# Kernel optimization log

Hardware: AMD Instinct MI355X
Metric: run time of the kernel (lower is better)

## Reference

```python
import jax, jax.numpy as jnp
import numpy as np

BELIEF = 1024
STOCH = 32
DISC = 32
LATENT = 1024
MLP = 1024
ACT = 6
B = 256
T = 64
UNIMIX = 0.01
FREE = 0.1
DYN_SCALE = 1.0
REP_SCALE = 0.1
EPS = 1e-8
SAMP_EPS = 1e-6
CLIP = 20.0
UPDATE_BIAS = -1.0


def _lin_init(key, fan_in, fan_out):
    return jax.random.normal(key, (fan_in, fan_out), jnp.float32) / np.sqrt(fan_in)


def setup_inputs() -> dict:
    key = jax.random.key(0)
    ks = jax.random.split(key, 16)
    inp = {
        "b0": jnp.zeros((B, BELIEF), jnp.float32),
        "z0": jax.random.uniform(ks[0], (B, STOCH * DISC), jnp.float32),
        "actions": jax.random.normal(ks[1], (T, B, ACT), jnp.float32),
        "obs": jax.random.normal(ks[2], (T, B, LATENT), jnp.float32),
        "u_noise": jax.random.uniform(ks[3], (T, B, STOCH, DISC), jnp.float32),
        # imagine_in MLP: (stoch*disc + act) -> MLP -> LATENT
        "Wi1": _lin_init(ks[4], STOCH * DISC + ACT, MLP),
        "bi1": jnp.zeros((MLP,), jnp.float32),
        "Wi2": _lin_init(ks[5], MLP, LATENT),
        "bi2": jnp.zeros((LATENT,), jnp.float32),
        # GRU linear: (LATENT + BELIEF) -> 3*BELIEF, no bias; LayerNorm(3*BELIEF, eps=1e-3)
        "Wg": _lin_init(ks[6], LATENT + BELIEF, 3 * BELIEF),
        "ln_scale": jnp.ones((3 * BELIEF,), jnp.float32),
        "ln_bias": jnp.zeros((3 * BELIEF,), jnp.float32),
        # posterior MLP: (LATENT + BELIEF) -> LATENT -> STOCH*DISC
        "Wo1": _lin_init(ks[7], LATENT + BELIEF, LATENT),
        "bo1": jnp.zeros((LATENT,), jnp.float32),
        "Wo2": _lin_init(ks[8], LATENT, STOCH * DISC),
        "bo2": jnp.zeros((STOCH * DISC,), jnp.float32),
        # prior (belief decoder) MLP: BELIEF -> LATENT -> STOCH*DISC
        "Wp1": _lin_init(ks[9], BELIEF, LATENT),
        "bp1": jnp.zeros((LATENT,), jnp.float32),
        "Wp2": _lin_init(ks[10], LATENT, STOCH * DISC),
        "bp2": jnp.zeros((STOCH * DISC,), jnp.float32),
    }
    return inp


def _mlp2(x, W1, b1, W2, b2):
    h = jax.nn.silu(x @ W1 + b1)
    return h @ W2 + b2


def _layernorm(x, scale, bias, eps=1e-3):
    mu = x.mean(-1, keepdims=True)
    var = ((x - mu) ** 2).mean(-1, keepdims=True)
    return (x - mu) / jnp.sqrt(var + eps) * scale + bias


def _probs_from_logits(logits_flat):
    # reshape (..., STOCH*DISC) -> (..., STOCH, DISC), clip, softmax, unimix
    logits = logits_flat.reshape(*logits_flat.shape[:-1], STOCH, DISC)
    logits = jnp.clip(logits, -CLIP, CLIP)
    probs = jax.nn.softmax(logits, axis=-1)
    probs = probs * (1.0 - UNIMIX) + UNIMIX / DISC
    return probs


def _kl_cate(post_probs, prior_probs):
    sg = jax.lax.stop_gradient
    log_post = jnp.log(post_probs + EPS)
    kl_rep = (post_probs * (log_post - jnp.log(sg(prior_probs) + EPS))).sum((-2, -1))
    kl_dyn = (sg(post_probs) * (sg(log_post) - jnp.log(prior_probs + EPS))).sum((-2, -1))
    rep_loss = jnp.maximum(kl_rep, FREE)
    dyn_loss = jnp.maximum(kl_dyn, FREE)
    return DYN_SCALE * dyn_loss + REP_SCALE * rep_loss


def reference(b0, z0, actions, obs, u_noise,
              Wi1, bi1, Wi2, bi2,
              Wg, ln_scale, ln_bias,
              Wo1, bo1, Wo2, bo2,
              Wp1, bp1, Wp2, bp2):
    def gru(inp, h):
        gates = _layernorm(jnp.concatenate([inp, h], axis=-1) @ Wg, ln_scale, ln_bias)
        r, c, u = jnp.split(gates, 3, axis=-1)
        reset = jax.nn.sigmoid(r)
        cand = jnp.tanh(reset * c)
        update = jax.nn.sigmoid(u + UPDATE_BIAS)
        return update * cand + (1.0 - update) * h

    def step(carry, xs):
        b, z = carry
        a_t, o_t, u_t = xs
        inp = _mlp2(jnp.concatenate([z, a_t], axis=-1), Wi1, bi1, Wi2, bi2)
        b_new = gru(inp, b)                                      # (B, BELIEF)
        prior_probs = _probs_from_logits(_mlp2(b_new, Wp1, bp1, Wp2, bp2))
        post_probs = _probs_from_logits(
            _mlp2(jnp.concatenate([o_t, b_new], axis=-1), Wo1, bo1, Wo2, bo2))
        # gumbel-max categorical sample + straight-through one-hot
        g = -jnp.log(-jnp.log(u_t + SAMP_EPS) + SAMP_EPS)
        logp = jnp.log(jnp.maximum(post_probs, SAMP_EPS))
        hard = jnp.argmax(logp + g, axis=-1)                     # (B, STOCH)
        y_hard = jax.nn.one_hot(hard, DISC, dtype=post_probs.dtype)
        z_st = y_hard + post_probs - jax.lax.stop_gradient(post_probs)
        z_flat = z_st.reshape(z_st.shape[0], STOCH * DISC)
        loss = _kl_cate(post_probs, prior_probs)                 # (B,)
        return (b_new, z_flat), loss

    (_, _), losses = jax.lax.scan(step, (b0, z0), (actions, obs, u_noise))
    return losses  # (T, B)
```

## Files before the change

kernel.cpp:

```cpp
#include <hip/hip_runtime.h>
#include <math.h>


typedef _Float16 f16;
typedef _Float16 f16x8 __attribute__((ext_vector_type(8)));
typedef float f32x4 __attribute__((ext_vector_type(4)));

constexpr int kB = 256, kN1 = 1024, kG3N = 3072, kActD = 6, kT = 64;
constexpr float kLoScale = 4096.f;
constexpr float kLoInv = 1.f / 4096.f;

__device__ __forceinline__ void wr_planes(f16* hi, f16* lo, size_t i, float x) {
  f16 h = (f16)x;
  hi[i] = h;
  lo[i] = (f16)((x - (float)h) * kLoScale);
}

__device__ __forceinline__ void glds16(const f16* g, f16* l) {
  __builtin_amdgcn_global_load_lds(
      (const __attribute__((address_space(1))) unsigned int*)g,
      (__attribute__((address_space(3))) unsigned int*)l, 16, 0, 0);
}

struct MJob {
  const f16 *A1h, *A1l, *A2h, *A2l;
  const f16 *Wph, *Wpl;
  float* outF;
  int cols1, K, Nout, k0, klen, ny;
};
struct MJobs { MJob j[6]; };

__global__ __launch_bounds__(256, 2) void k_mgemm(MJobs js) {
  const MJob jb = js.j[blockIdx.z];
  if ((int)blockIdx.y >= jb.ny) return;
  const int m0 = blockIdx.x * 128, n0 = blockIdx.y * 64;
  __shared__ __align__(16) f16 As[2][2][8][64][8];
  __shared__ __align__(16) f16 Ws[2][2][4][64][8];
  const int t = threadIdx.x, wave = t >> 6, lane = t & 63;
  const int rlo = lane & 15, khi = (lane >> 4) * 8;
  const int wmf = (wave & 1) * 4, wnf = (wave >> 1) * 2;

  f32x4 acc1[4][2], acc2[4][2];
#pragma unroll
  for (int i = 0; i < 4; ++i)
#pragma unroll
    for (int j = 0; j < 2; ++j)
#pragma unroll
      for (int r = 0; r < 4; ++r) { acc1[i][j][r] = 0.f; acc2[i][j][r] = 0.f; }

  auto issueTile = [&](int it, int buf) {
    const int kg = jb.k0 + it * 32;
    const f16 *h, *l; int rs, cb;
    if (kg < jb.cols1) { h = jb.A1h; l = jb.A1l; rs = jb.cols1; cb = kg; }
    else { h = jb.A2h; l = jb.A2l; rs = jb.K - jb.cols1; cb = kg - jb.cols1; }
#pragma unroll
    for (int i = 0; i < 2; ++i) {
      const int mf = wave * 2 + i;
      const size_t go = (size_t)(m0 + mf * 16 + rlo) * rs + cb + khi;
      glds16(h + go, &As[buf][0][mf][0][0]);
      glds16(l + go, &As[buf][1][mf][0][0]);
    }
    const size_t wo = (size_t)(n0 + wave * 16 + rlo) * jb.K + kg + khi;
    glds16(jb.Wph + wo, &Ws[buf][0][wave][0][0]);
    glds16(jb.Wpl + wo, &Ws[buf][1][wave][0][0]);
  };

  issueTile(0, 0);
  __syncthreads();
  const int niter = jb.klen >> 5;
  for (int it = 0; it < niter; ++it) {
    const int buf = it & 1;
    if (it + 1 < niter) issueTile(it + 1, buf ^ 1);
    f16x8 Af[4][2], Wf[2][2];
#pragma unroll
    for (int mf = 0; mf < 4; ++mf) {
      Af[mf][0] = *(const f16x8*)&As[buf][0][wmf + mf][lane][0];
      Af[mf][1] = *(const f16x8*)&As[buf][1][wmf + mf][lane][0];
    }
#pragma unroll
    for (int nf = 0; nf < 2; ++nf) {
      Wf[nf][0] = *(const f16x8*)&Ws[buf][0][wnf + nf][lane][0];
      Wf[nf][1] = *(const f16x8*)&Ws[buf][1][wnf + nf][lane][0];
    }
#pragma unroll
    for (int mf = 0; mf < 4; ++mf)
#pragma unroll
      for (int nf = 0; nf < 2; ++nf) {
        acc1[mf][nf] = __builtin_amdgcn_mfma_f32_16x16x32_f16(Af[mf][0], Wf[nf][0], acc1[mf][nf], 0, 0, 0);
        acc2[mf][nf] = __builtin_amdgcn_mfma_f32_16x16x32_f16(Af[mf][0], Wf[nf][1], acc2[mf][nf], 0, 0, 0);
        acc2[mf][nf] = __builtin_amdgcn_mfma_f32_16x16x32_f16(Af[mf][1], Wf[nf][0], acc2[mf][nf], 0, 0, 0);
      }
    __syncthreads();
  }
  const int orow = m0 + (wave & 1) * 64, ocol = n0 + (wave >> 1) * 32;
#pragma unroll
  for (int mf = 0; mf < 4; ++mf)
#pragma unroll
    for (int nf = 0; nf < 2; ++nf)
#pragma unroll
      for (int r = 0; r < 4; ++r) {
        const int row = orow + mf * 16 + (lane >> 4) * 4 + r;
        const int col = ocol + nf * 16 + rlo;
        jb.outF[(size_t)row * jb.Nout + col] = acc1[mf][nf][r] + acc2[mf][nf][r] * kLoInv;
      }
}

struct CJob { const float* P; int nparts; const float* bias; f16* oh; f16* ol; };
struct CJobs { CJob j[2]; };

__global__ __launch_bounds__(256) void k_comb(CJobs js) {
  const CJob jb = js.j[blockIdx.y];
  const int i = blockIdx.x * 256 + threadIdx.x;
  float s = 0.f;
  for (int p = 0; p < jb.nparts; ++p) s += jb.P[(size_t)p * (kB * kN1) + i];
  s += jb.bias[i & (kN1 - 1)];
  s = s * (1.f / (1.f + expf(-s)));
  wr_planes(jb.oh, jb.ol, i, s);
}

__global__ __launch_bounds__(256) void k_conv(const float* src, f16* dh, f16* dl) {
  const size_t i = (size_t)blockIdx.x * 256 + threadIdx.x;
  wr_planes(dh, dl, i, src[i]);
}

__global__ __launch_bounds__(256) void k_convT(const float* src, int rowoff, int srcN,
                                               int K, f16* dh, f16* dl) {
  __shared__ float T[64][65];
  const int k0 = blockIdx.x * 64, n0 = blockIdx.y * 64;
  const int tx = threadIdx.x & 63, ty = threadIdx.x >> 6;
#pragma unroll 4
  for (int i = 0; i < 16; ++i) {
    const int k = ty * 16 + i;
    T[k][tx] = src[(size_t)(rowoff + k0 + k) * srcN + n0 + tx];
  }
  __syncthreads();
#pragma unroll 4
  for (int i = 0; i < 16; ++i) {
    const int n = ty * 16 + i;
    const float x = T[tx][n];
    const size_t o = (size_t)(n0 + n) * K + k0 + tx;
    f16 h = (f16)x;
    dh[o] = h;
    dl[o] = (f16)((x - (float)h) * kLoScale);
  }
}

__global__ __launch_bounds__(256) void k_bfused(const float* Wg, const float* bi2, float* bf) {
  const int n = blockIdx.x * 256 + threadIdx.x;
  float s = 0.f;
  for (int j = 0; j < 1024; ++j) s += bi2[j] * Wg[(size_t)j * kG3N + n];
  bf[n] = s;
}

__global__ __launch_bounds__(256) void k_setup(const float* b0, float* bbuf, f16* bh, f16* bl) {
  const size_t i = (size_t)blockIdx.x * 256 + threadIdx.x;
  const float b = b0[i];
  bbuf[i] = b;
  wr_planes(bh, bl, i, b);
}

__global__ __launch_bounds__(256) void k_finish0(const float* P, const float* Wi1,
    const float* bi1, const float* act0, f16* h1h, f16* h1l) {
  const int b = blockIdx.y;
  const int j = blockIdx.x * 256 + threadIdx.x;
  __shared__ float sact[kActD];
  if (threadIdx.x < kActD) sact[threadIdx.x] = act0[b * kActD + threadIdx.x];
  __syncthreads();
  float s = P[(size_t)b * kN1 + j] + bi1[j];
#pragma unroll
  for (int k = 0; k < kActD; ++k) s += sact[k] * Wi1[(size_t)(kN1 + k) * kN1 + j];
  s = s * (1.f / (1.f + expf(-s)));
  wr_planes(h1h, h1l, (size_t)b * kN1 + j, s);
}

__global__ __launch_bounds__(256) void k_gru(const float* Pg, const float* bfused,
    const float* lns, const float* lnb, float* bbuf, f16* bh, f16* bl,
    const float* obs_next, f16* oh, f16* ol, int do_obs) {
  const int b = blockIdx.x;
  const int tid = threadIdx.x;
  const size_t S3 = (size_t)kB * kG3N;
  __shared__ float sh[kG3N];
  __shared__ float red[8];
  float v[12];
  float sum = 0.f, sq = 0.f;
#pragma unroll
  for (int i = 0; i < 12; ++i) {
    const int j = tid + i * 256;
    const size_t o = (size_t)b * kG3N + j;
    const float s = Pg[o] + Pg[S3 + o] + Pg[2 * S3 + o] + Pg[3 * S3 + o] + bfused[j];
    v[i] = s; sum += s; sq += s * s;
  }
  if (do_obs) {
#pragma unroll
    for (int i = 0; i < 4; ++i) {
      const int j = tid + i * 256;
      wr_planes(oh, ol, (size_t)b * kN1 + j, obs_next[(size_t)b * kN1 + j]);
    }
  }
  for (int m = 1; m <= 32; m <<= 1) { sum += __shfl_xor(sum, m); sq += __shfl_xor(sq, m); }
  if ((tid & 63) == 0) { red[(tid >> 6) * 2] = sum; red[(tid >> 6) * 2 + 1] = sq; }
  __syncthreads();
  float ts = 0.f, tq = 0.f;
  for (int w = 0; w < 4; ++w) { ts += red[w * 2]; tq += red[w * 2 + 1]; }
  const float mu   = ts * (1.f / kG3N);
  const float var  = tq * (1.f / kG3N) - mu * mu;
  const float rinv = 1.f / sqrtf(var + 1e-3f);
#pragma unroll
  for (int i = 0; i < 12; ++i) {
    const int j = tid + i * 256;
    sh[j] = (v[i] - mu) * rinv * lns[j] + lnb[j];
  }
  __syncthreads();
#pragma unroll
  for (int i = 0; i < 4; ++i) {
    const int j = tid + i * 256;
    const float r = sh[j], c = sh[kN1 + j], u = sh[2 * kN1 + j];
    const float reset = 1.f / (1.f + expf(-r));
    const float cand  = tanhf(reset * c);
    const float upd   = 1.f / (1.f + expf(-(u - 1.f)));
    const size_t o = (size_t)b * kN1 + j;
    const float bn = upd * cand + (1.f - upd) * bbuf[o];
    bbuf[o] = bn;
    wr_planes(bh, bl, o, bn);
  }
}

__global__ __launch_bounds__(1024) void k_sample(const float* PE,
    const float* bp2, const float* bo2, const float* unz_t, float* loss_t,
    const float* Wi1, const float* bi1, const float* act_next,
    f16* h1h, f16* h1l, int do_gather) {
  const int b = blockIdx.x;
  const int tid = threadIdx.x;
  const size_t PL = (size_t)kB * kN1;
  const size_t o = (size_t)b * kN1 + tid;
  float lp = PE[o] + PE[PL + o] + bp2[tid];
  float lo = PE[2 * PL + o] + PE[3 * PL + o] + bo2[tid];
  lp = fminf(fmaxf(lp, -20.f), 20.f);
  lo = fminf(fmaxf(lo, -20.f), 20.f);
  float mp = lp, mo = lo;
  for (int m = 1; m <= 16; m <<= 1) { mp = fmaxf(mp, __shfl_xor(mp, m)); mo = fmaxf(mo, __shfl_xor(mo, m)); }
  const float ep = expf(lp - mp), eo = expf(lo - mo);
  float sp = ep, so = eo;
  for (int m = 1; m <= 16; m <<= 1) { sp += __shfl_xor(sp, m); so += __shfl_xor(so, m); }
  const float pp = (ep / sp) * 0.99f + (0.01f / 32.f);
  const float po = (eo / so) * 0.99f + (0.01f / 32.f);
  float kt = po * (logf(po + 1e-8f) - logf(pp + 1e-8f));
  for (int m = 1; m <= 16; m <<= 1) kt += __shfl_xor(kt, m);
  const float u = unz_t[o];
  const float g = -logf(-logf(u + 1e-6f) + 1e-6f);
  float vv = logf(fmaxf(po, 1e-6f)) + g;
  int ii = tid & 31;
  for (int m = 1; m <= 16; m <<= 1) {
    const float vo = __shfl_xor(vv, m);
    const int   io = __shfl_xor(ii, m);
    if (vo > vv || (vo == vv && io < ii)) { vv = vo; ii = io; }
  }
  __shared__ float skl[32];
  __shared__ int   sidx[32];
  if ((tid & 31) == 0) { skl[tid >> 5] = kt; sidx[tid >> 5] = ii; }
  __syncthreads();
  if (tid == 0) {
    float kl = 0.f;
    for (int gg = 0; gg < 32; ++gg) kl += skl[gg];
    const float dl = fmaxf(kl, 0.1f);
    loss_t[b] = 1.0f * dl + 0.1f * dl;
  }
  if (do_gather) {
    float s = bi1[tid];
#pragma unroll
    for (int gg = 0; gg < 32; ++gg)
      s += Wi1[(size_t)(gg * 32 + sidx[gg]) * kN1 + tid];
#pragma unroll
    for (int k = 0; k < kActD; ++k)
      s += act_next[b * kActD + k] * Wi1[(size_t)(kN1 + k) * kN1 + tid];
    s = s * (1.f / (1.f + expf(-s)));
    wr_planes(h1h, h1l, o, s);
  }
}

extern "C" void kernel_launch(void* const* d_in, const int* in_sizes, int n_in,
                              void* d_out, int out_size, void* d_ws, size_t ws_size,
                              hipStream_t stream) {
  const float* b0   = (const float*)d_in[0];
  const float* z0   = (const float*)d_in[1];
  const float* acts = (const float*)d_in[2];
  const float* obs  = (const float*)d_in[3];
  const float* unz  = (const float*)d_in[4];
  const float* Wi1  = (const float*)d_in[5];
  const float* bi1  = (const float*)d_in[6];
  const float* Wi2  = (const float*)d_in[7];
  const float* bi2  = (const float*)d_in[8];
  const float* Wg   = (const float*)d_in[9];
  const float* lns  = (const float*)d_in[10];
  const float* lnb  = (const float*)d_in[11];
  const float* Wo1  = (const float*)d_in[12];
  const float* bo1  = (const float*)d_in[13];
  const float* Wo2  = (const float*)d_in[14];
  const float* bo2  = (const float*)d_in[15];
  const float* Wp1  = (const float*)d_in[16];
  const float* bp1  = (const float*)d_in[17];
  const float* Wp2  = (const float*)d_in[18];
  const float* bp2  = (const float*)d_in[19];
  float* out = (float*)d_out;

  char* wsb = (char*)d_ws;
  size_t off = 0;
  auto allocB = [&](size_t bytes) { char* p = wsb + off; off += (bytes + 255) & ~(size_t)255; return p; };
  const size_t PL = (size_t)kB * kN1;
  const size_t S3 = (size_t)kB * kG3N;
  const size_t W1 = (size_t)kN1 * kN1;

  float* Pg = (float*)allocB(4 * S3 * 4);
  float* Wfused_tmp = Pg;
  f16* WgTh = (f16*)allocB(W1 * 3 * 2);
  f16* WgTl = (f16*)allocB(W1 * 3 * 2);
  float* PD = (float*)WgTh;
  float* PE = (float*)WgTl;
  f16* h1h = (f16*)allocB(PL * 2);  f16* h1l = (f16*)allocB(PL * 2);
  f16* bh  = (f16*)allocB(PL * 2);  f16* bl  = (f16*)allocB(PL * 2);
  f16* hph = (f16*)allocB(PL * 2);  f16* hpl = (f16*)allocB(PL * 2);
  f16* hoh = (f16*)allocB(PL * 2);  f16* hol = (f16*)allocB(PL * 2);
  f16* o0h = (f16*)allocB(PL * 2);  f16* o0l = (f16*)allocB(PL * 2);
  f16* o1h = (f16*)allocB(PL * 2);  f16* o1l = (f16*)allocB(PL * 2);
  f16* z0h = (f16*)allocB(PL * 2);  f16* z0l = (f16*)allocB(PL * 2);
  float* bbuf   = (float*)allocB(PL * 4);
  float* bfused = (float*)allocB((size_t)kG3N * 4);
  f16* WfTh = (f16*)allocB(W1 * 3 * 2);  f16* WfTl = (f16*)allocB(W1 * 3 * 2);
  f16* WgBh = (f16*)allocB(W1 * 3 * 2);  f16* WgBl = (f16*)allocB(W1 * 3 * 2);
  f16* Wi2h = (f16*)allocB(W1 * 2);      f16* Wi2l = (f16*)allocB(W1 * 2);
  f16* Wi1Th = (f16*)allocB(W1 * 2);     f16* Wi1Tl = (f16*)allocB(W1 * 2);
  f16* Wo1Th = (f16*)allocB(W1 * 2 * 2); f16* Wo1Tl = (f16*)allocB(W1 * 2 * 2);
  f16* Wp1Th = (f16*)allocB(W1 * 2);     f16* Wp1Tl = (f16*)allocB(W1 * 2);
  f16* Wp2Th = (f16*)allocB(W1 * 2);     f16* Wp2Tl = (f16*)allocB(W1 * 2);
  f16* Wo2Th = (f16*)allocB(W1 * 2);     f16* Wo2Tl = (f16*)allocB(W1 * 2);

  k_convT<<<dim3(16, 48), 256, 0, stream>>>(Wg, 0, kG3N, 1024, WgTh, WgTl);
  k_convT<<<dim3(16, 48), 256, 0, stream>>>(Wg, 1024, kG3N, 1024, WgBh, WgBl);
  k_convT<<<dim3(16, 16), 256, 0, stream>>>(Wi1, 0, kN1, 1024, Wi1Th, Wi1Tl);
  k_convT<<<dim3(32, 16), 256, 0, stream>>>(Wo1, 0, kN1, 2048, Wo1Th, Wo1Tl);
  k_convT<<<dim3(16, 16), 256, 0, stream>>>(Wp1, 0, kN1, 1024, Wp1Th, Wp1Tl);
  k_convT<<<dim3(16, 16), 256, 0, stream>>>(Wp2, 0, kN1, 1024, Wp2Th, Wp2Tl);
  k_convT<<<dim3(16, 16), 256, 0, stream>>>(Wo2, 0, kN1, 1024, Wo2Th, Wo2Tl);
  k_conv<<<dim3(4096), 256, 0, stream>>>(Wi2, Wi2h, Wi2l);
  k_bfused<<<dim3(12), 256, 0, stream>>>(Wg, bi2, bfused);
  {
    MJobs J{};
    J.j[0] = { Wi2h, Wi2l, nullptr, nullptr, WgTh, WgTl, Wfused_tmp, 1024, 1024, kG3N, 0, 1024, 48 };
    k_mgemm<<<dim3(8, 48, 1), 256, 0, stream>>>(J);
  }
  k_convT<<<dim3(16, 48), 256, 0, stream>>>(Wfused_tmp, 0, kG3N, 1024, WfTh, WfTl);
  k_setup<<<dim3(1024), 256, 0, stream>>>(b0, bbuf, bh, bl);
  k_conv<<<dim3(1024), 256, 0, stream>>>(z0, z0h, z0l);
  k_conv<<<dim3(1024), 256, 0, stream>>>(obs, o0h, o0l);
  {
    MJobs J{};
    J.j[0] = { z0h, z0l, nullptr, nullptr, Wi1Th, Wi1Tl, PD, 1024, 1024, kN1, 0, 1024, 16 };
    k_mgemm<<<dim3(2, 16, 1), 256, 0, stream>>>(J);
  }
  k_finish0<<<dim3(4, kB), 256, 0, stream>>>(PD, Wi1, bi1, acts, h1h, h1l);

  for (int t = 0; t < kT; ++t) {
    const float* unz_t = unz + (size_t)t * kB * kN1;
    f16* oth = (t & 1) ? o1h : o0h;
    f16* otl = (t & 1) ? o1l : o0l;
    f16* onh = (t & 1) ? o0h : o1h;
    f16* onl = (t & 1) ? o0l : o1l;

    {
      MJobs J{};
      J.j[0] = { h1h, h1l, nullptr, nullptr, WfTh, WfTl, Pg,          1024, 1024, kG3N, 0,   512, 48 };
      J.j[1] = { h1h, h1l, nullptr, nullptr, WfTh, WfTl, Pg + S3,     1024, 1024, kG3N, 512, 512, 48 };
      J.j[2] = { bh,  bl,  nullptr, nullptr, WgBh, WgBl, Pg + 2 * S3, 1024, 1024, kG3N, 0,   512, 48 };
      J.j[3] = { bh,  bl,  nullptr, nullptr, WgBh, WgBl, Pg + 3 * S3, 1024, 1024, kG3N, 512, 512, 48 };
      k_mgemm<<<dim3(2, 48, 4), 256, 0, stream>>>(J);
    }
    k_gru<<<dim3(kB), 256, 0, stream>>>(Pg, bfused, lns, lnb, bbuf, bh, bl,
                                        obs + (size_t)(t + 1) * kB * kN1, onh, onl,
                                        (t < kT - 1) ? 1 : 0);
    {
      MJobs J{};
      J.j[0] = { bh,  bl,  nullptr, nullptr, Wp1Th, Wp1Tl, PD,          1024, 1024, kN1, 0,    512, 16 };
      J.j[1] = { bh,  bl,  nullptr, nullptr, Wp1Th, Wp1Tl, PD + PL,     1024, 1024, kN1, 512,  512, 16 };
      J.j[2] = { oth, otl, bh, bl,           Wo1Th, Wo1Tl, PD + 2 * PL, 1024, 2048, kN1, 0,    512, 16 };
      J.j[3] = { oth, otl, bh, bl,           Wo1Th, Wo1Tl, PD + 3 * PL, 1024, 2048, kN1, 512,  512, 16 };
      J.j[4] = { oth, otl, bh, bl,           Wo1Th, Wo1Tl, PD + 4 * PL, 1024, 2048, kN1, 1024, 512, 16 };
      J.j[5] = { oth, otl, bh, bl,           Wo1Th, Wo1Tl, PD + 5 * PL, 1024, 2048, kN1, 1536, 512, 16 };
      k_mgemm<<<dim3(2, 16, 6), 256, 0, stream>>>(J);
    }
    {
      CJobs C{};
      C.j[0] = { PD,          2, bp1, hph, hpl };
      C.j[1] = { PD + 2 * PL, 4, bo1, hoh, hol };
      k_comb<<<dim3(1024, 2), 256, 0, stream>>>(C);
    }
    {
      MJobs J{};
      J.j[0] = { hph, hpl, nullptr, nullptr, Wp2Th, Wp2Tl, PE,          1024, 1024, kN1, 0,   512, 16 };
      J.j[1] = { hph, hpl, nullptr, nullptr, Wp2Th, Wp2Tl, PE + PL,     1024, 1024, kN1, 512, 512, 16 };
      J.j[2] = { hoh, hol, nullptr, nullptr, Wo2Th, Wo2Tl, PE + 2 * PL, 1024, 1024, kN1, 0,   512, 16 };
      J.j[3] = { hoh, hol, nullptr, nullptr, Wo2Th, Wo2Tl, PE + 3 * PL, 1024, 1024, kN1, 512, 512, 16 };
      k_mgemm<<<dim3(2, 16, 4), 256, 0, stream>>>(J);
    }
    k_sample<<<dim3(kB), 1024, 0, stream>>>(PE, bp2, bo2, unz_t,
                                            out + (size_t)t * kB,
                                            Wi1, bi1, acts + (size_t)(t + 1) * kB * kActD,
                                            h1h, h1l, (t < kT - 1) ? 1 : 0);
  }
}
```

Baseline: 5.980 ms.

## Fuse the per-timestep kernel sequence into one persistent kernel with grid barriers

Replaces the 64×6 per-step kernel launches (GEMMs, GRU, combine, sample) with a single persistent kernel. Its blocks loop over tasks for each stage and meet at a software grid-wide barrier built on an atomic counter. This removes launch overhead and inter-kernel gaps, and the block count is sized from occupancy. The cost is a spin barrier that needs every block co-resident, with a guard timeout that could silently break ordering. The sample stage now runs with 256 threads per batch row instead of 1024.

```diff
diff --git a/kernel.cpp b/kernel.cpp
--- a/kernel.cpp
+++ b/kernel.cpp
@@ -20,6 +20,304 @@
   __builtin_amdgcn_global_load_lds(
       (const __attribute__((address_space(1))) unsigned int*)g,
       (__attribute__((address_space(3))) unsigned int*)l, 16, 0, 0);
+}
+
+struct GemmLDS { f16 As[2][2][8][64][8]; f16 Ws[2][2][4][64][8]; };
+struct GruLDS  { float sh[kG3N]; float red[8]; };
+struct SmpLDS  { float skl[32]; int sidx[32]; };
+union ScanLDS  { GemmLDS g; GruLDS r; SmpLDS s; };
+
+__device__ void dev_mgemm(GemmLDS& L, const f16* A1h, const f16* A1l,
+                          const f16* A2h, const f16* A2l,
+                          const f16* Wph, const f16* Wpl, float* outF,
+                          int cols1, int K, int Nout, int k0, int klen,
+                          int bx, int by) {
+  const int m0 = bx * 128, n0 = by * 64;
+  const int tid = threadIdx.x, wave = tid >> 6, lane = tid & 63;
+  const int rlo = lane & 15, khi = (lane >> 4) * 8;
+  const int wmf = (wave & 1) * 4, wnf = (wave >> 1) * 2;
+
+  f32x4 acc1[4][2], acc2[4][2];
+#pragma unroll
+  for (int i = 0; i < 4; ++i)
+#pragma unroll
+    for (int j = 0; j < 2; ++j)
+#pragma unroll
+      for (int r = 0; r < 4; ++r) { acc1[i][j][r] = 0.f; acc2[i][j][r] = 0.f; }
+
+  auto issueTile = [&](int it, int buf) {
+    const int kg = k0 + it * 32;
+    const f16 *h, *l; int rs, cb;
+    if (kg < cols1) { h = A1h; l = A1l; rs = cols1; cb = kg; }
+    else { h = A2h; l = A2l; rs = K - cols1; cb = kg - cols1; }
+#pragma unroll
+    for (int i = 0; i < 2; ++i) {
+      const int mf = wave * 2 + i;
+      const size_t go = (size_t)(m0 + mf * 16 + rlo) * rs + cb + khi;
+      glds16(h + go, &L.As[buf][0][mf][0][0]);
+      glds16(l + go, &L.As[buf][1][mf][0][0]);
+    }
+    const size_t wo = (size_t)(n0 + wave * 16 + rlo) * K + kg + khi;
+    glds16(Wph + wo, &L.Ws[buf][0][wave][0][0]);
+    glds16(Wpl + wo, &L.Ws[buf][1][wave][0][0]);
+  };
+
+  issueTile(0, 0);
+  __syncthreads();
+  const int niter = klen >> 5;
+#pragma unroll 1
+  for (int it = 0; it < niter; ++it) {
+    const int buf = it & 1;
+    if (it + 1 < niter) issueTile(it + 1, buf ^ 1);
+    f16x8 Af[4][2], Wf[2][2];
+#pragma unroll
+    for (int mf = 0; mf < 4; ++mf) {
+      Af[mf][0] = *(const f16x8*)&L.As[buf][0][wmf + mf][lane][0];
+      Af[mf][1] = *(const f16x8*)&L.As[buf][1][wmf + mf][lane][0];
+    }
+#pragma unroll
+    for (int nf = 0; nf < 2; ++nf) {
+      Wf[nf][0] = *(const f16x8*)&L.Ws[buf][0][wnf + nf][lane][0];
+      Wf[nf][1] = *(const f16x8*)&L.Ws[buf][1][wnf + nf][lane][0];
+    }
+#pragma unroll
+    for (int mf = 0; mf < 4; ++mf)
+#pragma unroll
+      for (int nf = 0; nf < 2; ++nf) {
+        acc1[mf][nf] = __builtin_amdgcn_mfma_f32_16x16x32_f16(Af[mf][0], Wf[nf][0], acc1[mf][nf], 0, 0, 0);
+        acc2[mf][nf] = __builtin_amdgcn_mfma_f32_16x16x32_f16(Af[mf][0], Wf[nf][1], acc2[mf][nf], 0, 0, 0);
+        acc2[mf][nf] = __builtin_amdgcn_mfma_f32_16x16x32_f16(Af[mf][1], Wf[nf][0], acc2[mf][nf], 0, 0, 0);
+      }
+    __syncthreads();
+  }
+  const int orow = m0 + (wave & 1) * 64, ocol = n0 + (wave >> 1) * 32;
+#pragma unroll
+  for (int mf = 0; mf < 4; ++mf)
+#pragma unroll
+    for (int nf = 0; nf < 2; ++nf)
+#pragma unroll
+      for (int r = 0; r < 4; ++r) {
+        const int row = orow + mf * 16 + (lane >> 4) * 4 + r;
+        const int col = ocol + nf * 16 + rlo;
+        outF[(size_t)row * Nout + col] = acc1[mf][nf][r] + acc2[mf][nf][r] * kLoInv;
+      }
+}
+
+__device__ void dev_gru(GruLDS& G, int b, const float* Pg, const float* bfused,
+                        const float* lns, const float* lnb, float* bbuf,
+                        f16* bh, f16* bl, const float* obs_next,
+                        f16* oh, f16* ol, int do_obs) {
+  const int tid = threadIdx.x;
+  const size_t S3 = (size_t)kB * kG3N;
+  float v[12];
+  float sum = 0.f, sq = 0.f;
+#pragma unroll
+  for (int i = 0; i < 12; ++i) {
+    const int j = tid + i * 256;
+    const size_t o = (size_t)b * kG3N + j;
+    const float s = Pg[o] + Pg[S3 + o] + Pg[2 * S3 + o] + Pg[3 * S3 + o] + bfused[j];
+    v[i] = s; sum += s; sq += s * s;
+  }
+  if (do_obs) {
+#pragma unroll
+    for (int i = 0; i < 4; ++i) {
+      const int j = tid + i * 256;
+      wr_planes(oh, ol, (size_t)b * kN1 + j, obs_next[(size_t)b * kN1 + j]);
+    }
+  }
+  for (int m = 1; m <= 32; m <<= 1) { sum += __shfl_xor(sum, m); sq += __shfl_xor(sq, m); }
+  if ((tid & 63) == 0) { G.red[(tid >> 6) * 2] = sum; G.red[(tid >> 6) * 2 + 1] = sq; }
+  __syncthreads();
+  float ts = 0.f, tq = 0.f;
+  for (int w = 0; w < 4; ++w) { ts += G.red[w * 2]; tq += G.red[w * 2 + 1]; }
+  const float mu   = ts * (1.f / kG3N);
+  const float var  = tq * (1.f / kG3N) - mu * mu;
+  const float rinv = 1.f / sqrtf(var + 1e-3f);
+#pragma unroll
+  for (int i = 0; i < 12; ++i) {
+    const int j = tid + i * 256;
+    G.sh[j] = (v[i] - mu) * rinv * lns[j] + lnb[j];
+  }
+  __syncthreads();
+#pragma unroll
+  for (int i = 0; i < 4; ++i) {
+    const int j = tid + i * 256;
+    const float r = G.sh[j], c = G.sh[kN1 + j], u = G.sh[2 * kN1 + j];
+    const float reset = 1.f / (1.f + expf(-r));
+    const float cand  = tanhf(reset * c);
+    const float upd   = 1.f / (1.f + expf(-(u - 1.f)));
+    const size_t o = (size_t)b * kN1 + j;
+    const float bn = upd * cand + (1.f - upd) * bbuf[o];
+    bbuf[o] = bn;
+    wr_planes(bh, bl, o, bn);
+  }
+}
+
+__device__ void dev_sample(SmpLDS& S, int b, const float* PE,
+                           const float* bp2, const float* bo2,
+                           const float* unz_t, float* loss_t,
+                           const float* Wi1, const float* bi1,
+                           const float* act_next, f16* h1h, f16* h1l,
+                           int do_gather) {
+  const int tid = threadIdx.x;
+  const size_t PL = (size_t)kB * kN1;
+  __syncthreads();
+#pragma unroll
+  for (int c = 0; c < 4; ++c) {
+    const int j = c * 256 + tid;
+    const size_t o = (size_t)b * kN1 + j;
+    float lp = PE[o] + PE[PL + o] + bp2[j];
+    float lo = PE[2 * PL + o] + PE[3 * PL + o] + bo2[j];
+    lp = fminf(fmaxf(lp, -20.f), 20.f);
+    lo = fminf(fmaxf(lo, -20.f), 20.f);
+    float mp = lp, mo = lo;
+    for (int m = 1; m <= 16; m <<= 1) { mp = fmaxf(mp, __shfl_xor(mp, m)); mo = fmaxf(mo, __shfl_xor(mo, m)); }
+    const float ep = expf(lp - mp), eo = expf(lo - mo);
+    float sp = ep, so = eo;
+    for (int m = 1; m <= 16; m <<= 1) { sp += __shfl_xor(sp, m); so += __shfl_xor(so, m); }
+    const float pp = (ep / sp) * 0.99f + (0.01f / 32.f);
+    const float po = (eo / so) * 0.99f + (0.01f / 32.f);
+    float kt = po * (logf(po + 1e-8f) - logf(pp + 1e-8f));
+    for (int m = 1; m <= 16; m <<= 1) kt += __shfl_xor(kt, m);
+    const float u = unz_t[o];
+    const float g = -logf(-logf(u + 1e-6f) + 1e-6f);
+    float vv = logf(fmaxf(po, 1e-6f)) + g;
+    int ii = j & 31;
+    for (int m = 1; m <= 16; m <<= 1) {
+      const float vo = __shfl_xor(vv, m);
+      const int   io = __shfl_xor(ii, m);
+      if (vo > vv || (vo == vv && io < ii)) { vv = vo; ii = io; }
+    }
+    if ((tid & 31) == 0) { S.skl[j >> 5] = kt; S.sidx[j >> 5] = ii; }
+  }
+  __syncthreads();
+  if (tid == 0) {
+    float kl = 0.f;
+    for (int gg = 0; gg < 32; ++gg) kl += S.skl[gg];
+    const float dl = fmaxf(kl, 0.1f);
+    loss_t[b] = 1.0f * dl + 0.1f * dl;
+  }
+  if (do_gather) {
+#pragma unroll
+    for (int c = 0; c < 4; ++c) {
+      const int j = c * 256 + tid;
+      float s = bi1[j];
+#pragma unroll
+      for (int gg = 0; gg < 32; ++gg)
+        s += Wi1[(size_t)(gg * 32 + S.sidx[gg]) * kN1 + j];
+#pragma unroll
+      for (int k = 0; k < kActD; ++k)
+        s += act_next[b * kActD + k] * Wi1[(size_t)(kN1 + k) * kN1 + j];
+      s = s * (1.f / (1.f + expf(-s)));
+      wr_planes(h1h, h1l, (size_t)b * kN1 + j, s);
+    }
+  }
+}
+
+struct ScanArgs {
+  const float *obs, *acts, *unz;
+  float* out;
+  const float *lns, *lnb, *bp1, *bo1, *bp2, *bo2, *Wi1, *bi1;
+  float *Pg, *PD, *PE, *bbuf, *bfused;
+  const f16 *WfTh, *WfTl, *WgBh, *WgBl;
+  const f16 *Wp1Th, *Wp1Tl, *Wo1Th, *Wo1Tl, *Wp2Th, *Wp2Tl, *Wo2Th, *Wo2Tl;
+  f16 *h1h, *h1l, *bh, *bl, *hph, *hpl, *hoh, *hol, *o0h, *o0l, *o1h, *o1l;
+  int* cnt;
+  int NB;
+};
+
+__device__ __forceinline__ void gsync_impl(int* cnt, int tgt) {
+  __syncthreads();
+  if (threadIdx.x == 0) {
+    __threadfence();
+    __hip_atomic_fetch_add(cnt, 1, __ATOMIC_RELEASE, __HIP_MEMORY_SCOPE_AGENT);
+    int guard = 0;
+    while (__hip_atomic_load(cnt, __ATOMIC_RELAXED, __HIP_MEMORY_SCOPE_AGENT) < tgt) {
+      __builtin_amdgcn_s_sleep(2);
+      if (++guard > (1 << 26)) break;
+    }
+    __threadfence();
+  }
+  __syncthreads();
+}
+
+__global__ __launch_bounds__(256, 2) void k_scan(ScanArgs a) {
+  __shared__ ScanLDS L;
+  const int NB = a.NB;
+  const size_t PL = (size_t)kB * kN1;
+  const size_t S3 = (size_t)kB * kG3N;
+  int syncno = 0;
+
+#pragma unroll 1
+  for (int t = 0; t < kT; ++t) {
+    const f16* oth = (t & 1) ? a.o1h : a.o0h;
+    const f16* otl = (t & 1) ? a.o1l : a.o0l;
+    f16* onh = (t & 1) ? a.o0h : a.o1h;
+    f16* onl = (t & 1) ? a.o0l : a.o1l;
+
+#pragma unroll 1
+    for (int task = blockIdx.x; task < 384; task += NB) {
+      const int j = task / 96, r = task % 96, bx = r & 1, by = r >> 1;
+      const bool top = (j < 2);
+      dev_mgemm(L.g, top ? a.h1h : a.bh, top ? a.h1l : a.bl, nullptr, nullptr,
+                top ? a.WfTh : a.WgBh, top ? a.WfTl : a.WgBl,
+                a.Pg + (size_t)j * S3, 1024, 1024, kG3N, (j & 1) * 512, 512, bx, by);
+    }
+    gsync_impl(a.cnt, ++syncno * NB);
+
+#pragma unroll 1
+    for (int b = blockIdx.x; b < kB; b += NB)
+      dev_gru(L.r, b, a.Pg, a.bfused, a.lns, a.lnb, a.bbuf, a.bh, a.bl,
+              a.obs + (size_t)(t + 1) * kB * kN1, onh, onl, (t < kT - 1) ? 1 : 0);
+    gsync_impl(a.cnt, ++syncno * NB);
+
+#pragma unroll 1
+    for (int task = blockIdx.x; task < 192; task += NB) {
+      const int j = task >> 5, r = task & 31, bx = r & 1, by = r >> 1;
+      const f16 *Ah, *Al, *A2h = nullptr, *A2l = nullptr, *Wh, *Wl;
+      int K, k0;
+      if (j < 2) { Ah = a.bh; Al = a.bl; Wh = a.Wp1Th; Wl = a.Wp1Tl; K = 1024; k0 = j * 512; }
+      else { Ah = oth; Al = otl; A2h = a.bh; A2l = a.bl; Wh = a.Wo1Th; Wl = a.Wo1Tl; K = 2048; k0 = (j - 2) * 512; }
+      dev_mgemm(L.g, Ah, Al, A2h, A2l, Wh, Wl,
+                a.PD + (size_t)j * PL, 1024, K, kN1, k0, 512, bx, by);
+    }
+    gsync_impl(a.cnt, ++syncno * NB);
+
+#pragma unroll 1
+    for (int idx = blockIdx.x; idx < 2048; idx += NB) {
+      const int by = idx >> 10;
+      const int i = (idx & 1023) * 256 + (int)threadIdx.x;
+      const float* P = by ? (a.PD + 2 * PL) : a.PD;
+      const int np = by ? 4 : 2;
+      const float* bias = by ? a.bo1 : a.bp1;
+      f16* oh = by ? a.hoh : a.hph;
+      f16* ol = by ? a.hol : a.hpl;
+      float s = 0.f;
+      for (int p = 0; p < np; ++p) s += P[(size_t)p * PL + i];
+      s += bias[i & (kN1 - 1)];
+      s = s * (1.f / (1.f + expf(-s)));
+      wr_planes(oh, ol, i, s);
+    }
+    gsync_impl(a.cnt, ++syncno * NB);
+
+#pragma unroll 1
+    for (int task = blockIdx.x; task < 128; task += NB) {
+      const int j = task >> 5, r = task & 31, bx = r & 1, by = r >> 1;
+      const bool pr = (j < 2);
+      dev_mgemm(L.g, pr ? a.hph : a.hoh, pr ? a.hpl : a.hol, nullptr, nullptr,
+                pr ? a.Wp2Th : a.Wo2Th, pr ? a.Wp2Tl : a.Wo2Tl,
+                a.PE + (size_t)j * PL, 1024, 1024, kN1, (j & 1) * 512, 512, bx, by);
+    }
+    gsync_impl(a.cnt, ++syncno * NB);
+
+#pragma unroll 1
+    for (int b = blockIdx.x; b < kB; b += NB)
+      dev_sample(L.s, b, a.PE, a.bp2, a.bo2, a.unz + (size_t)t * PL,
+                 a.out + (size_t)t * kB, a.Wi1, a.bi1,
+                 a.acts + (size_t)(t + 1) * kB * kActD, a.h1h, a.h1l,
+                 (t < kT - 1) ? 1 : 0);
+    gsync_impl(a.cnt, ++syncno * NB);
+  }
 }
 
 struct MJob {
@@ -33,89 +331,9 @@
 __global__ __launch_bounds__(256, 2) void k_mgemm(MJobs js) {
   const MJob jb = js.j[blockIdx.z];
   if ((int)blockIdx.y >= jb.ny) return;
-  const int m0 = blockIdx.x * 128, n0 = blockIdx.y * 64;
-  __shared__ __align__(16) f16 As[2][2][8][64][8];
-  __shared__ __align__(16) f16 Ws[2][2][4][64][8];
-  const int t = threadIdx.x, wave = t >> 6, lane = t & 63;
-  const int rlo = lane & 15, khi = (lane >> 4) * 8;
-  const int wmf = (wave & 1) * 4, wnf = (wave >> 1) * 2;
-
-  f32x4 acc1[4][2], acc2[4][2];
-#pragma unroll
-  for (int i = 0; i < 4; ++i)
-#pragma unroll
-    for (int j = 0; j < 2; ++j)
-#pragma unroll
-      for (int r = 0; r < 4; ++r) { acc1[i][j][r] = 0.f; acc2[i][j][r] = 0.f; }
-
-  auto issueTile = [&](int it, int buf) {
-    const int kg = jb.k0 + it * 32;
-    const f16 *h, *l; int rs, cb;
-    if (kg < jb.cols1) { h = jb.A1h; l = jb.A1l; rs = jb.cols1; cb = kg; }
-    else { h = jb.A2h; l = jb.A2l; rs = jb.K - jb.cols1; cb = kg - jb.cols1; }
-#pragma unroll
-    for (int i = 0; i < 2; ++i) {
-      const int mf = wave * 2 + i;
-      const size_t go = (size_t)(m0 + mf * 16 + rlo) * rs + cb + khi;
-      glds16(h + go, &As[buf][0][mf][0][0]);
-      glds16(l + go, &As[buf][1][mf][0][0]);
-    }
-    const size_t wo = (size_t)(n0 + wave * 16 + rlo) * jb.K + kg + khi;
-    glds16(jb.Wph + wo, &Ws[buf][0][wave][0][0]);
-    glds16(jb.Wpl + wo, &Ws[buf][1][wave][0][0]);
-  };
-
-  issueTile(0, 0);
-  __syncthreads();
-  const int niter = jb.klen >> 5;
-  for (int it = 0; it < niter; ++it) {
-    const int buf = it & 1;
-    if (it + 1 < niter) issueTile(it + 1, buf ^ 1);
-    f16x8 Af[4][2], Wf[2][2];
-#pragma unroll
-    for (int mf = 0; mf < 4; ++mf) {
-      Af[mf][0] = *(const f16x8*)&As[buf][0][wmf + mf][lane][0];
-      Af[mf][1] = *(const f16x8*)&As[buf][1][wmf + mf][lane][0];
-    }
-#pragma unroll
-    for (int nf = 0; nf < 2; ++nf) {
-      Wf[nf][0] = *(const f16x8*)&Ws[buf][0][wnf + nf][lane][0];
-      Wf[nf][1] = *(const f16x8*)&Ws[buf][1][wnf + nf][lane][0];
-    }
-#pragma unroll
-    for (int mf = 0; mf < 4; ++mf)
-#pragma unroll
-      for (int nf = 0; nf < 2; ++nf) {
-        acc1[mf][nf] = __builtin_amdgcn_mfma_f32_16x16x32_f16(Af[mf][0], Wf[nf][0], acc1[mf][nf], 0, 0, 0);
-        acc2[mf][nf] = __builtin_amdgcn_mfma_f32_16x16x32_f16(Af[mf][0], Wf[nf][1], acc2[mf][nf], 0, 0, 0);
-        acc2[mf][nf] = __builtin_amdgcn_mfma_f32_16x16x32_f16(Af[mf][1], Wf[nf][0], acc2[mf][nf], 0, 0, 0);
-      }
-    __syncthreads();
-  }
-  const int orow = m0 + (wave & 1) * 64, ocol = n0 + (wave >> 1) * 32;
-#pragma unroll
-  for (int mf = 0; mf < 4; ++mf)
-#pragma unroll
-    for (int nf = 0; nf < 2; ++nf)
-#pragma unroll
-      for (int r = 0; r < 4; ++r) {
-        const int row = orow + mf * 16 + (lane >> 4) * 4 + r;
-        const int col = ocol + nf * 16 + rlo;
-        jb.outF[(size_t)row * jb.Nout + col] = acc1[mf][nf][r] + acc2[mf][nf][r] * kLoInv;
-      }
-}
-
-struct CJob { const float* P; int nparts; const float* bias; f16* oh; f16* ol; };
-struct CJobs { CJob j[2]; };
-
-__global__ __launch_bounds__(256) void k_comb(CJobs js) {
-  const CJob jb = js.j[blockIdx.y];
-  const int i = blockIdx.x * 256 + threadIdx.x;
-  float s = 0.f;
-  for (int p = 0; p < jb.nparts; ++p) s += jb.P[(size_t)p * (kB * kN1) + i];
-  s += jb.bias[i & (kN1 - 1)];
-  s = s * (1.f / (1.f + expf(-s)));
-  wr_planes(jb.oh, jb.ol, i, s);
+  __shared__ GemmLDS L;
+  dev_mgemm(L, jb.A1h, jb.A1l, jb.A2h, jb.A2l, jb.Wph, jb.Wpl, jb.outF,
+            jb.cols1, jb.K, jb.Nout, jb.k0, jb.klen, blockIdx.x, blockIdx.y);
 }
 
 __global__ __launch_bounds__(256) void k_conv(const float* src, f16* dh, f16* dl) {
@@ -159,6 +377,10 @@
   wr_planes(bh, bl, i, b);
 }
 
+__global__ void k_zero(int* p) {
+  if (threadIdx.x == 0 && blockIdx.x == 0) *p = 0;
+}
+
 __global__ __launch_bounds__(256) void k_finish0(const float* P, const float* Wi1,
     const float* bi1, const float* act0, f16* h1h, f16* h1l) {
   const int b = blockIdx.y;
@@ -171,111 +393,6 @@
   for (int k = 0; k < kActD; ++k) s += sact[k] * Wi1[(size_t)(kN1 + k) * kN1 + j];
   s = s * (1.f / (1.f + expf(-s)));
   wr_planes(h1h, h1l, (size_t)b * kN1 + j, s);
-}
-
-__global__ __launch_bounds__(256) void k_gru(const float* Pg, const float* bfused,
-    const float* lns, const float* lnb, float* bbuf, f16* bh, f16* bl,
-    const float* obs_next, f16* oh, f16* ol, int do_obs) {
-  const int b = blockIdx.x;
-  const int tid = threadIdx.x;
-  const size_t S3 = (size_t)kB * kG3N;
-  __shared__ float sh[kG3N];
-  __shared__ float red[8];
-  float v[12];
-  float sum = 0.f, sq = 0.f;
-#pragma unroll
-  for (int i = 0; i < 12; ++i) {
-    const int j = tid + i * 256;
-    const size_t o = (size_t)b * kG3N + j;
-    const float s = Pg[o] + Pg[S3 + o] + Pg[2 * S3 + o] + Pg[3 * S3 + o] + bfused[j];
-    v[i] = s; sum += s; sq += s * s;
-  }
-  if (do_obs) {
-#pragma unroll
-    for (int i = 0; i < 4; ++i) {
-      const int j = tid + i * 256;
-      wr_planes(oh, ol, (size_t)b * kN1 + j, obs_next[(size_t)b * kN1 + j]);
-    }
-  }
-  for (int m = 1; m <= 32; m <<= 1) { sum += __shfl_xor(sum, m); sq += __shfl_xor(sq, m); }
-  if ((tid & 63) == 0) { red[(tid >> 6) * 2] = sum; red[(tid >> 6) * 2 + 1] = sq; }
-  __syncthreads();
-  float ts = 0.f, tq = 0.f;
-  for (int w = 0; w < 4; ++w) { ts += red[w * 2]; tq += red[w * 2 + 1]; }
-  const float mu   = ts * (1.f / kG3N);
-  const float var  = tq * (1.f / kG3N) - mu * mu;
-  const float rinv = 1.f / sqrtf(var + 1e-3f);
-#pragma unroll
-  for (int i = 0; i < 12; ++i) {
-    const int j = tid + i * 256;
-    sh[j] = (v[i] - mu) * rinv * lns[j] + lnb[j];
-  }
-  __syncthreads();
-#pragma unroll
-  for (int i = 0; i < 4; ++i) {
-    const int j = tid + i * 256;
-    const float r = sh[j], c = sh[kN1 + j], u = sh[2 * kN1 + j];
-    const float reset = 1.f / (1.f + expf(-r));
-    const float cand  = tanhf(reset * c);
-    const float upd   = 1.f / (1.f + expf(-(u - 1.f)));
-    const size_t o = (size_t)b * kN1 + j;
-    const float bn = upd * cand + (1.f - upd) * bbuf[o];
-    bbuf[o] = bn;
-    wr_planes(bh, bl, o, bn);
-  }
-}
-
-__global__ __launch_bounds__(1024) void k_sample(const float* PE,
-    const float* bp2, const float* bo2, const float* unz_t, float* loss_t,
-    const float* Wi1, const float* bi1, const float* act_next,
-    f16* h1h, f16* h1l, int do_gather) {
-  const int b = blockIdx.x;
-  const int tid = threadIdx.x;
-  const size_t PL = (size_t)kB * kN1;
-  const size_t o = (size_t)b * kN1 + tid;
-  float lp = PE[o] + PE[PL + o] + bp2[tid];
-  float lo = PE[2 * PL + o] + PE[3 * PL + o] + bo2[tid];
-  lp = fminf(fmaxf(lp, -20.f), 20.f);
-  lo = fminf(fmaxf(lo, -20.f), 20.f);
-  float mp = lp, mo = lo;
-  for (int m = 1; m <= 16; m <<= 1) { mp = fmaxf(mp, __shfl_xor(mp, m)); mo = fmaxf(mo, __shfl_xor(mo, m)); }
-  const float ep = expf(lp - mp), eo = expf(lo - mo);
-  float sp = ep, so = eo;
-  for (int m = 1; m <= 16; m <<= 1) { sp += __shfl_xor(sp, m); so += __shfl_xor(so, m); }
-  const float pp = (ep / sp) * 0.99f + (0.01f / 32.f);
-  const float po = (eo / so) * 0.99f + (0.01f / 32.f);
-  float kt = po * (logf(po + 1e-8f) - logf(pp + 1e-8f));
-  for (int m = 1; m <= 16; m <<= 1) kt += __shfl_xor(kt, m);
-  const float u = unz_t[o];
-  const float g = -logf(-logf(u + 1e-6f) + 1e-6f);
-  float vv = logf(fmaxf(po, 1e-6f)) + g;
-  int ii = tid & 31;
-  for (int m = 1; m <= 16; m <<= 1) {
-    const float vo = __shfl_xor(vv, m);
-    const int   io = __shfl_xor(ii, m);
-    if (vo > vv || (vo == vv && io < ii)) { vv = vo; ii = io; }
-  }
-  __shared__ float skl[32];
-  __shared__ int   sidx[32];
-  if ((tid & 31) == 0) { skl[tid >> 5] = kt; sidx[tid >> 5] = ii; }
-  __syncthreads();
-  if (tid == 0) {
-    float kl = 0.f;
-    for (int gg = 0; gg < 32; ++gg) kl += skl[gg];
-    const float dl = fmaxf(kl, 0.1f);
-    loss_t[b] = 1.0f * dl + 0.1f * dl;
-  }
-  if (do_gather) {
-    float s = bi1[tid];
-#pragma unroll
-    for (int gg = 0; gg < 32; ++gg)
-      s += Wi1[(size_t)(gg * 32 + sidx[gg]) * kN1 + tid];
-#pragma unroll
-    for (int k = 0; k < kActD; ++k)
-      s += act_next[b * kActD + k] * Wi1[(size_t)(kN1 + k) * kN1 + tid];
-    s = s * (1.f / (1.f + expf(-s)));
-    wr_planes(h1h, h1l, o, s);
-  }
 }
 
 extern "C" void kernel_launch(void* const* d_in, const int* in_sizes, int n_in,
@@ -333,6 +450,24 @@
   f16* Wp1Th = (f16*)allocB(W1 * 2);     f16* Wp1Tl = (f16*)allocB(W1 * 2);
   f16* Wp2Th = (f16*)allocB(W1 * 2);     f16* Wp2Tl = (f16*)allocB(W1 * 2);
   f16* Wo2Th = (f16*)allocB(W1 * 2);     f16* Wo2Tl = (f16*)allocB(W1 * 2);
+  int* cnt = (int*)allocB(256);
+
+  static int s_nb = 0;
+  if (s_nb == 0) {
+    int dev = 0;
+    (void)hipGetDevice(&dev);
+    int cu = 0;
+    if (hipDeviceGetAttribute(&cu, hipDeviceAttributeMultiprocessorCount, dev) != hipSuccess || cu <= 0)
+      cu = 256;
+    int occ = 0;
+    if (hipOccupancyMaxActiveBlocksPerMultiprocessor(&occ, k_scan, 256, 0) != hipSuccess || occ < 1)
+      occ = 1;
+    long nb = (long)occ * (long)cu;
+    if (nb > 512) nb = 512;
+    if (nb < 64) nb = 64;
+    s_nb = (int)nb;
+  }
+  const int NB = s_nb;
 
   k_convT<<<dim3(16, 48), 256, 0, stream>>>(Wg, 0, kG3N, 1024, WgTh, WgTl);
   k_convT<<<dim3(16, 48), 256, 0, stream>>>(Wg, 1024, kG3N, 1024, WgBh, WgBl);
@@ -352,6 +487,7 @@
   k_setup<<<dim3(1024), 256, 0, stream>>>(b0, bbuf, bh, bl);
   k_conv<<<dim3(1024), 256, 0, stream>>>(z0, z0h, z0l);
   k_conv<<<dim3(1024), 256, 0, stream>>>(obs, o0h, o0l);
+  k_zero<<<dim3(1), 64, 0, stream>>>(cnt);
   {
     MJobs J{};
     J.j[0] = { z0h, z0l, nullptr, nullptr, Wi1Th, Wi1Tl, PD, 1024, 1024, kN1, 0, 1024, 16 };
@@ -359,51 +495,17 @@
   }
   k_finish0<<<dim3(4, kB), 256, 0, stream>>>(PD, Wi1, bi1, acts, h1h, h1l);
 
-  for (int t = 0; t < kT; ++t) {
-    const float* unz_t = unz + (size_t)t * kB * kN1;
-    f16* oth = (t & 1) ? o1h : o0h;
-    f16* otl = (t & 1) ? o1l : o0l;
-    f16* onh = (t & 1) ? o0h : o1h;
-    f16* onl = (t & 1) ? o0l : o1l;
-
-    {
-      MJobs J{};
-      J.j[0] = { h1h, h1l, nullptr, nullptr, WfTh, WfTl, Pg,          1024, 1024, kG3N, 0,   512, 48 };
-      J.j[1] = { h1h, h1l, nullptr, nullptr, WfTh, WfTl, Pg + S3,     1024, 1024, kG3N, 512, 512, 48 };
-      J.j[2] = { bh,  bl,  nullptr, nullptr, WgBh, WgBl, Pg + 2 * S3, 1024, 1024, kG3N, 0,   512, 48 };
-      J.j[3] = { bh,  bl,  nullptr, nullptr, WgBh, WgBl, Pg + 3 * S3, 1024, 1024, kG3N, 512, 512, 48 };
-      k_mgemm<<<dim3(2, 48, 4), 256, 0, stream>>>(J);
-    }
-    k_gru<<<dim3(kB), 256, 0, stream>>>(Pg, bfused, lns, lnb, bbuf, bh, bl,
-                                        obs + (size_t)(t + 1) * kB * kN1, onh, onl,
-                                        (t < kT - 1) ? 1 : 0);
-    {
-      MJobs J{};
-      J.j[0] = { bh,  bl,  nullptr, nullptr, Wp1Th, Wp1Tl, PD,          1024, 1024, kN1, 0,    512, 16 };
-      J.j[1] = { bh,  bl,  nullptr, nullptr, Wp1Th, Wp1Tl, PD + PL,     1024, 1024, kN1, 512,  512, 16 };
-      J.j[2] = { oth, otl, bh, bl,           Wo1Th, Wo1Tl, PD + 2 * PL, 1024, 2048, kN1, 0,    512, 16 };
-      J.j[3] = { oth, otl, bh, bl,           Wo1Th, Wo1Tl, PD + 3 * PL, 1024, 2048, kN1, 512,  512, 16 };
-      J.j[4] = { oth, otl, bh, bl,           Wo1Th, Wo1Tl, PD + 4 * PL, 1024, 2048, kN1, 1024, 512, 16 };
-      J.j[5] = { oth, otl, bh, bl,           Wo1Th, Wo1Tl, PD + 5 * PL, 1024, 2048, kN1, 1536, 512, 16 };
-      k_mgemm<<<dim3(2, 16, 6), 256, 0, stream>>>(J);
-    }
-    {
-      CJobs C{};
-      C.j[0] = { PD,          2, bp1, hph, hpl };
-      C.j[1] = { PD + 2 * PL, 4, bo1, hoh, hol };
-      k_comb<<<dim3(1024, 2), 256, 0, stream>>>(C);
-    }
-    {
-      MJobs J{};
-      J.j[0] = { hph, hpl, nullptr, nullptr, Wp2Th, Wp2Tl, PE,          1024, 1024, kN1, 0,   512, 16 };
-      J.j[1] = { hph, hpl, nullptr, nullptr, Wp2Th, Wp2Tl, PE + PL,     1024, 1024, kN1, 512, 512, 16 };
-      J.j[2] = { hoh, hol, nullptr, nullptr, Wo2Th, Wo2Tl, PE + 2 * PL, 1024, 1024, kN1, 0,   512, 16 };
-      J.j[3] = { hoh, hol, nullptr, nullptr, Wo2Th, Wo2Tl, PE + 3 * PL, 1024, 1024, kN1, 512, 512, 16 };
-      k_mgemm<<<dim3(2, 16, 4), 256, 0, stream>>>(J);
-    }
-    k_sample<<<dim3(kB), 1024, 0, stream>>>(PE, bp2, bo2, unz_t,
-                                            out + (size_t)t * kB,
-                                            Wi1, bi1, acts + (size_t)(t + 1) * kB * kActD,
-                                            h1h, h1l, (t < kT - 1) ? 1 : 0);
-  }
-}
+  ScanArgs A;
+  A.obs = obs; A.acts = acts; A.unz = unz; A.out = out;
+  A.lns = lns; A.lnb = lnb; A.bp1 = bp1; A.bo1 = bo1; A.bp2 = bp2; A.bo2 = bo2;
+  A.Wi1 = Wi1; A.bi1 = bi1;
+  A.Pg = Pg; A.PD = PD; A.PE = PE; A.bbuf = bbuf; A.bfused = bfused;
+  A.WfTh = WfTh; A.WfTl = WfTl; A.WgBh = WgBh; A.WgBl = WgBl;
+  A.Wp1Th = Wp1Th; A.Wp1Tl = Wp1Tl; A.Wo1Th = Wo1Th; A.Wo1Tl = Wo1Tl;
+  A.Wp2Th = Wp2Th; A.Wp2Tl = Wp2Tl; A.Wo2Th = Wo2Th; A.Wo2Tl = Wo2Tl;
+  A.h1h = h1h; A.h1l = h1l; A.bh = bh; A.bl = bl;
+  A.hph = hph; A.hpl = hpl; A.hoh = hoh; A.hol = hol;
+  A.o0h = o0h; A.o0l = o0l; A.o1h = o1h; A.o1l = o1l;
+  A.cnt = cnt; A.NB = NB;
+  k_scan<<<dim3(NB), dim3(256), 0, stream>>>(A);
+}
```

Result: slower. 19.04 ms (+218.4%).
